# Performance work log

Measured on AMD Instinct MI355X. Metric: run time of the kernel, lower is better.

Reference implementation:

```python
import jax, jax.numpy as jnp
import numpy as np
from jax import lax

B, T, D, U = 128, 1024, 256, 48


def setup_inputs() -> dict:
    key = jax.random.key(0)
    k1, k2, k3 = jax.random.split(key, 3)
    x = jax.random.normal(k1, (B, T, D), dtype=jnp.float32)
    kernel = jax.random.normal(k2, (D, U), dtype=jnp.float32) * (1.0 / np.sqrt(D))
    bias = jnp.zeros((U,), dtype=jnp.float32)
    chain_kernel = jax.random.normal(k3, (U, U), dtype=jnp.float32)
    return {"x": x, "kernel": kernel, "bias": bias, "chain_kernel": chain_kernel}


def _viterbi_decode(logits, trans):
    # logits: [B, T, U], trans: [U, U]; full-length sequences (mask=None)
    init_state = logits[:, 0]  # [B, U]
    steps = jnp.swapaxes(logits[:, 1:], 0, 1)  # [T-1, B, U]

    def fwd(state, logit_t):
        # scores[b, i, j] = state[b, i] + trans[i, j]
        scores = state[:, :, None] + trans[None]  # [B, U, U]
        bp = jnp.argmax(scores, axis=1)            # [B, U] best prev tag
        new_state = logit_t + jnp.max(scores, axis=1)
        return new_state, bp

    final_state, bps = lax.scan(fwd, init_state, steps)  # bps: [T-1, B, U]
    last_tag = jnp.argmax(final_state, axis=-1)          # [B]

    def back(tag, bp):
        prev = jnp.take_along_axis(bp, tag[:, None], axis=1)[:, 0]
        return prev, prev

    # reverse scan emits tags for t = 0..T-2 in forward time order
    _, tags_head = lax.scan(back, last_tag, bps, reverse=True)  # [T-1, B]
    tags = jnp.concatenate([tags_head, last_tag[None]], axis=0)  # [T, B]
    return jnp.transpose(tags)  # [B, T]


def reference(x, kernel, bias, chain_kernel):
    # _dense_layer: linear activation -> x @ kernel + bias
    logits = jnp.einsum('btd,du->btu', x, kernel) + bias  # [B, T, U]
    pred_ids = _viterbi_decode(logits, chain_kernel)       # [B, T] int
    return pred_ids.astype(jnp.float32)
```

## Files before the change

### kernel.cpp

```cpp
#include <hip/hip_runtime.h>
#include <cstdint>

#define B_ 128
#define T_ 1024
#define D_ 256
#define U_ 48

typedef float v2f __attribute__((ext_vector_type(2)));

__device__ __forceinline__ v2f pk_add(v2f a, v2f b) {
    v2f d;
    asm("v_pk_add_f32 %0, %1, %2" : "=v"(d) : "v"(a), "v"(b));
    return d;
}
__device__ __forceinline__ float max3f(float a, float b, float c) {
    float d;
    asm("v_max3_f32 %0, %1, %2, %3" : "=v"(d) : "v"(a), "v"(b), "v"(c));
    return d;
}

__global__ __launch_bounds__(256, 1) void k_logits(const float* __restrict__ x,
                                                   const float* __restrict__ kern,
                                                   const float* __restrict__ bias,
                                                   float* __restrict__ logits) {
    __shared__ float K[D_ * U_];
    __shared__ float bsh[U_];
    const int tid = threadIdx.x;
    for (int i = tid; i < D_ * U_; i += 256) K[i] = kern[i];
    if (tid < U_) bsh[tid] = bias[tid];
    __syncthreads();

    const long row0 = (long)blockIdx.x * 256 + tid;
    const long row1 = row0 + (long)B_ * T_ / 2;
    const float4* xr0 = (const float4*)(x + row0 * D_);
    const float4* xr1 = (const float4*)(x + row1 * D_);

    float a0[U_], a1[U_];
#pragma unroll
    for (int u = 0; u < U_; ++u) { a0[u] = 0.0f; a1[u] = 0.0f; }

#pragma unroll 1
    for (int blk = 0; blk < D_ / 32; ++blk) {
        float4 xa[8], xb[8];
#pragma unroll
        for (int i = 0; i < 8; ++i) xa[i] = xr0[blk * 8 + i];
#pragma unroll
        for (int i = 0; i < 8; ++i) xb[i] = xr1[blk * 8 + i];

#pragma unroll
        for (int i = 0; i < 8; ++i) {
            const int d4 = blk * 8 + i;
            const float xc0[4] = {xa[i].x, xa[i].y, xa[i].z, xa[i].w};
            const float xc1[4] = {xb[i].x, xb[i].y, xb[i].z, xb[i].w};
#pragma unroll
            for (int c = 0; c < 4; ++c) {
                const float4* kp = (const float4*)&K[(d4 * 4 + c) * U_];
                const float s0 = xc0[c], s1 = xc1[c];
#pragma unroll
                for (int u4 = 0; u4 < U_ / 4; ++u4) {
                    float4 kv = kp[u4];
                    a0[u4*4+0] += s0 * kv.x;  a1[u4*4+0] += s1 * kv.x;
                    a0[u4*4+1] += s0 * kv.y;  a1[u4*4+1] += s1 * kv.y;
                    a0[u4*4+2] += s0 * kv.z;  a1[u4*4+2] += s1 * kv.z;
                    a0[u4*4+3] += s0 * kv.w;  a1[u4*4+3] += s1 * kv.w;
                }
            }
        }
    }

    float4* o0 = (float4*)(logits + row0 * U_);
    float4* o1 = (float4*)(logits + row1 * U_);
#pragma unroll
    for (int i = 0; i < U_ / 4; ++i) {
        float4 v0, v1;
        v0.x = a0[i*4+0] + bsh[i*4+0];  v1.x = a1[i*4+0] + bsh[i*4+0];
        v0.y = a0[i*4+1] + bsh[i*4+1];  v1.y = a1[i*4+1] + bsh[i*4+1];
        v0.z = a0[i*4+2] + bsh[i*4+2];  v1.z = a1[i*4+2] + bsh[i*4+2];
        v0.w = a0[i*4+3] + bsh[i*4+3];  v1.w = a1[i*4+3] + bsh[i*4+3];
        o0[i] = v0;
        o1[i] = v1;
    }
}

__device__ __forceinline__ float step_max_lds(const float4* sb, const v2f* tc2) {
    float4 s[12];
#pragma unroll
    for (int k = 0; k < 12; ++k) s[k] = sb[k];
    float cf[48];
#pragma unroll
    for (int k = 0; k < 12; ++k) {
        v2f lo, hi;
        lo.x = s[k].x; lo.y = s[k].y;
        hi.x = s[k].z; hi.y = s[k].w;
        v2f r0 = pk_add(lo, tc2[2 * k + 0]);
        v2f r1 = pk_add(hi, tc2[2 * k + 1]);
        cf[4*k+0] = r0.x; cf[4*k+1] = r0.y;
        cf[4*k+2] = r1.x; cf[4*k+3] = r1.y;
    }
    float t1[16];
#pragma unroll
    for (int i = 0; i < 16; ++i) t1[i] = max3f(cf[3*i], cf[3*i+1], cf[3*i+2]);
    float t2[6];
#pragma unroll
    for (int i = 0; i < 5; ++i) t2[i] = max3f(t1[3*i], t1[3*i+1], t1[3*i+2]);
    t2[5] = t1[15];
    const float a = max3f(t2[0], t2[1], t2[2]);
    const float b = max3f(t2[3], t2[4], t2[5]);
    return fmaxf(a, b);
}

__global__ __launch_bounds__(64, 1) void k_forward(const float* __restrict__ trans,
                                                   const float* __restrict__ logits,
                                                   float* __restrict__ delta) {
    __shared__ float4 sbuf[2][U_ / 4];
    const int lane = threadIdx.x;
    const int b = blockIdx.x;
    const int u = (lane < U_) ? lane : (U_ - 1);

    v2f tc2[U_ / 2];
#pragma unroll
    for (int v = 0; v < U_; v += 2) {
        tc2[v / 2].x = trans[v * U_ + u];
        tc2[v / 2].y = trans[(v + 1) * U_ + u];
    }

    const float* lin = logits + (long)b * T_ * U_;
    float* dout = delta + (long)b * T_ * U_;

    float state = lin[u];
    dout[u] = state;
    ((float*)sbuf[0])[u] = state;

    float pf[8];
#pragma unroll
    for (int i = 0; i < 8; ++i) pf[i] = lin[(1 + i) * U_ + u];

    const float* lp = lin + 9 * U_ + u;
    float* dp = dout + 1 * U_ + u;

#pragma unroll 1
    for (int g = 0; g < 127; ++g) {
#pragma unroll
        for (int j = 0; j < 8; ++j) {
            const float logit = pf[j];
            pf[j] = lp[j * U_];

            const float4* sb = sbuf[j & 1];
            const float m = step_max_lds(sb, tc2);
            state = logit + m;
            ((float*)sbuf[(j & 1) ^ 1])[u] = state;
            dp[j * U_] = state;
        }
        lp += 8 * U_;
        dp += 8 * U_;
    }

#pragma unroll
    for (int j = 0; j < 7; ++j) {
        const float logit = pf[j];
        const float4* sb = sbuf[j & 1];
        const float m = step_max_lds(sb, tc2);
        state = logit + m;
        ((float*)sbuf[(j & 1) ^ 1])[u] = state;
        dp[j * U_] = state;
    }
}

__global__ __launch_bounds__(64, 1) void k_forward_inplace(const float* __restrict__ trans,
                                                           float* __restrict__ delta) {
    __shared__ float4 sbuf[2][U_ / 4];
    const int lane = threadIdx.x;
    const int b = blockIdx.x;
    const int u = (lane < U_) ? lane : (U_ - 1);

    v2f tc2[U_ / 2];
#pragma unroll
    for (int v = 0; v < U_; v += 2) {
        tc2[v / 2].x = trans[v * U_ + u];
        tc2[v / 2].y = trans[(v + 1) * U_ + u];
    }

    float* base = delta + (long)b * T_ * U_;
    float state = base[u];
    ((float*)sbuf[0])[u] = state;

#pragma unroll 1
    for (int t = 1; t < T_; ++t) {
        const float logit = base[(long)t * U_ + u];
        const float m = step_max_lds(sbuf[(t - 1) & 1], tc2);
        state = logit + m;
        ((float*)sbuf[t & 1])[u] = state;
        base[(long)t * U_ + u] = state;
    }
}

#define BP_ROWS 32
__global__ __launch_bounds__(64, 1) void k_bp(const float* __restrict__ trans,
                                              const float* __restrict__ delta,
                                              unsigned char* __restrict__ bp) {
    __shared__ float sbuf[2][U_];
    const int lane = threadIdx.x;
    const int u = (lane < U_) ? lane : (U_ - 1);

    float tc[U_];
#pragma unroll
    for (int v = 0; v < U_; ++v) tc[v] = trans[v * U_ + u];

    const int NROW = B_ * (T_ - 1);
    const int row0 = blockIdx.x * BP_ROWS;
    if (row0 >= NROW) return;

    int b = row0 / (T_ - 1);
    int tm1 = row0 - b * (T_ - 1);

    float dval = delta[((long)b * T_ + tm1) * U_ + u];

#pragma unroll 1
    for (int i = 0; i < BP_ROWS; ++i) {
        const int row = row0 + i;
        if (row >= NROW) break;

        sbuf[i & 1][u] = dval;

        int bn = b, tn = tm1 + 1;
        if (tn == T_ - 1) { tn = 0; bn = b + 1; }
        float dnext = 0.0f;
        if (row + 1 < NROW) dnext = delta[((long)bn * T_ + tn) * U_ + u];

        const float4* sb4 = (const float4*)sbuf[i & 1];
        float best = -3.4e38f;
        int bi = 0;
#pragma unroll
        for (int k = 0; k < U_ / 4; ++k) {
            float4 s = sb4[k];
            float c0 = s.x + tc[4*k+0];
            float c1 = s.y + tc[4*k+1];
            float c2 = s.z + tc[4*k+2];
            float c3 = s.w + tc[4*k+3];
            bi = (c0 > best) ? 4*k+0 : bi;  best = fmaxf(best, c0);
            bi = (c1 > best) ? 4*k+1 : bi;  best = fmaxf(best, c1);
            bi = (c2 > best) ? 4*k+2 : bi;  best = fmaxf(best, c2);
            bi = (c3 > best) ? 4*k+3 : bi;  best = fmaxf(best, c3);
        }
        bp[(long)row * U_ + u] = (unsigned char)bi;

        b = bn; tm1 = tn; dval = dnext;
    }
}

#define KB_ 32
#define NB_ 32
__global__ __launch_bounds__(256) void k_back(const float* __restrict__ delta,
                                              const unsigned char* __restrict__ bp,
                                              float* __restrict__ out) {
    __shared__ unsigned char bpl[1024 * U_];
    __shared__ unsigned char gmap[NB_ * U_];
    __shared__ unsigned char eIn[NB_];
    __shared__ float tags[T_];
    __shared__ int Ash;
    const int tid = threadIdx.x;
    const int b = blockIdx.x;

    const uint32_t* src = (const uint32_t*)(bp + (long)b * (T_ - 1) * U_);
    uint32_t* dst = (uint32_t*)bpl;
    const int NW = (T_ - 1) * U_ / 4;
    for (int i = tid; i < NW; i += 256) dst[i] = src[i];
    if (tid < U_) bpl[1023 * U_ + tid] = (unsigned char)tid;

    if (tid < 64) {
        const int lane = tid;
        float v = (lane < U_) ? delta[((long)b * T_ + (T_ - 1)) * U_ + lane] : -3.4e38f;
        int idx = (lane < U_) ? lane : 64;
#pragma unroll
        for (int off = 32; off >= 1; off >>= 1) {
            const float ov = __shfl_xor(v, off);
            const int oi = __shfl_xor(idx, off);
            if (ov > v || (ov == v && oi < idx)) { v = ov; idx = oi; }
        }
        if (lane == 0) Ash = idx;
    }
    __syncthreads();

    int ik[6], ek[6], ck[6];
#pragma unroll
    for (int k = 0; k < 6; ++k) {
        const int tau = tid + k * 256;
        ik[k] = tau / U_;
        ek[k] = tau - ik[k] * U_;
        ck[k] = ek[k];
    }
#pragma unroll
    for (int h = 0; h < KB_; ++h) {
#pragma unroll
        for (int k = 0; k < 6; ++k) {
            const int r = ik[k] * KB_ + (KB_ - 1 - h);
            ck[k] = bpl[r * U_ + ck[k]];
        }
    }
#pragma unroll
    for (int k = 0; k < 6; ++k) gmap[ik[k] * U_ + ek[k]] = (unsigned char)ck[k];
    __syncthreads();

    if (tid == 0) {
        int cur = Ash;
        eIn[NB_ - 1] = (unsigned char)cur;
#pragma unroll 1
        for (int i = NB_ - 1; i >= 1; --i) {
            cur = gmap[i * U_ + cur];
            eIn[i - 1] = (unsigned char)cur;
        }
    }
    __syncthreads();

    if (tid < NB_) {
        const int i = tid;
        int cur = eIn[i];
#pragma unroll
        for (int h = 0; h < KB_; ++h) {
            const int r = i * KB_ + (KB_ - 1 - h);
            cur = bpl[r * U_ + cur];
            tags[r] = (float)cur;
        }
    }
    __syncthreads();

    float* o = out + (long)b * T_;
    for (int i = tid; i < T_; i += 256) o[i] = tags[i];
}

extern "C" void kernel_launch(void* const* d_in, const int* in_sizes, int n_in,
                              void* d_out, int out_size, void* d_ws, size_t ws_size,
                              hipStream_t stream) {
    const float* x     = (const float*)d_in[0];
    const float* kern  = (const float*)d_in[1];
    const float* bias  = (const float*)d_in[2];
    const float* trans = (const float*)d_in[3];
    float* out = (float*)d_out;

    const size_t NBT = (size_t)B_ * T_ * U_ * sizeof(float);

    float* logits = (float*)d_ws;
    const bool two_buf = ws_size >= 2 * NBT + (size_t)B_ * T_ * U_;
    float* delta = two_buf ? (float*)((char*)d_ws + NBT) : logits;
    unsigned char* bp = (unsigned char*)d_ws + (two_buf ? 2 * NBT : NBT);

    const int NROW = B_ * (T_ - 1);
    const int bp_grid = (NROW + BP_ROWS - 1) / BP_ROWS;

    k_logits<<<(B_ * T_ / 2) / 256, 256, 0, stream>>>(x, kern, bias, logits);
    if (two_buf)
        k_forward<<<B_, 64, 0, stream>>>(trans, logits, delta);
    else
        k_forward_inplace<<<B_, 64, 0, stream>>>(trans, logits);
    k_bp  <<<bp_grid, 64, 0, stream>>>(trans, delta, bp);
    k_back<<<B_, 256, 0, stream>>>(delta, bp, out);
}
```

Measured before the change: 500.4 us.

## Fuse forward recursion, backpointer computation and backtrace into one kernel

Replaces the separate forward, backpointer and backtrace kernels with one kernel per batch row. One wavefront runs the max-plus recursion and writes states into a 64-row LDS ring buffer, while a second wavefront computes argmax backpointers for the previous 32-step batch straight into LDS. This removes the global delta and bp round trips and two launches. The cost is a block barrier every 32 steps on the serial chain and only 128 blocks with 128 threads each doing the backpointer work.

Result: slower. 689.2 us (+37.7%).

```diff
diff --git a/kernel.cpp b/kernel.cpp
--- a/kernel.cpp
+++ b/kernel.cpp
@@ -109,167 +109,122 @@
     return fmaxf(a, b);
 }
 
-__global__ __launch_bounds__(64, 1) void k_forward(const float* __restrict__ trans,
-                                                   const float* __restrict__ logits,
-                                                   float* __restrict__ delta) {
-    __shared__ float4 sbuf[2][U_ / 4];
-    const int lane = threadIdx.x;
+#define RING 64
+#define BATCH 32
+
+#define CHAIN_STEP(IDX, J, DOPF)                                            \
+    {                                                                       \
+        const float logit = pf[IDX];                                        \
+        if (DOPF) pf[IDX] = lp[(J) * U_];                                   \
+        const float m = step_max_lds((const float4*)(ringf + roff), tc2);   \
+        state = logit + m;                                                  \
+        uint32_t woff = roff + U_;                                          \
+        woff = (woff >= (uint32_t)(RING * U_)) ? 0u : woff;                 \
+        ringf[woff + u] = state;                                            \
+        roff = woff;                                                        \
+    }
+
+#define CHAIN_GROUP8(PHI, DOPF)                                             \
+    CHAIN_STEP(((PHI) + 0) & 7, 0, DOPF)                                    \
+    CHAIN_STEP(((PHI) + 1) & 7, 1, DOPF)                                    \
+    CHAIN_STEP(((PHI) + 2) & 7, 2, DOPF)                                    \
+    CHAIN_STEP(((PHI) + 3) & 7, 3, DOPF)                                    \
+    CHAIN_STEP(((PHI) + 4) & 7, 4, DOPF)                                    \
+    CHAIN_STEP(((PHI) + 5) & 7, 5, DOPF)                                    \
+    CHAIN_STEP(((PHI) + 6) & 7, 6, DOPF)                                    \
+    CHAIN_STEP(((PHI) + 7) & 7, 7, DOPF)                                    \
+    lp += 8 * U_;
+
+__global__ __launch_bounds__(128, 1) void k_fused(const float* __restrict__ trans,
+                                                  const float* __restrict__ logits,
+                                                  float* __restrict__ out) {
+    __shared__ float ringf[RING * U_];
+    __shared__ unsigned char bpl[1024 * U_];
+    __shared__ unsigned char gmap[32 * U_];
+    __shared__ unsigned char eIn[32];
+    __shared__ int Ash;
+
+    const int tid = threadIdx.x;
+    const int wid = tid >> 6;
+    const int lane = tid & 63;
     const int b = blockIdx.x;
     const int u = (lane < U_) ? lane : (U_ - 1);
 
+    const float* lin = logits + (long)b * T_ * U_;
+
     v2f tc2[U_ / 2];
-#pragma unroll
-    for (int v = 0; v < U_; v += 2) {
-        tc2[v / 2].x = trans[v * U_ + u];
-        tc2[v / 2].y = trans[(v + 1) * U_ + u];
-    }
-
-    const float* lin = logits + (long)b * T_ * U_;
-    float* dout = delta + (long)b * T_ * U_;
-
-    float state = lin[u];
-    dout[u] = state;
-    ((float*)sbuf[0])[u] = state;
-
-    float pf[8];
-#pragma unroll
-    for (int i = 0; i < 8; ++i) pf[i] = lin[(1 + i) * U_ + u];
-
+    float state = 0.0f, pf[8];
     const float* lp = lin + 9 * U_ + u;
-    float* dp = dout + 1 * U_ + u;
-
-#pragma unroll 1
-    for (int g = 0; g < 127; ++g) {
-#pragma unroll
-        for (int j = 0; j < 8; ++j) {
-            const float logit = pf[j];
-            pf[j] = lp[j * U_];
-
-            const float4* sb = sbuf[j & 1];
-            const float m = step_max_lds(sb, tc2);
-            state = logit + m;
-            ((float*)sbuf[(j & 1) ^ 1])[u] = state;
-            dp[j * U_] = state;
-        }
-        lp += 8 * U_;
-        dp += 8 * U_;
-    }
-
-#pragma unroll
-    for (int j = 0; j < 7; ++j) {
-        const float logit = pf[j];
-        const float4* sb = sbuf[j & 1];
-        const float m = step_max_lds(sb, tc2);
-        state = logit + m;
-        ((float*)sbuf[(j & 1) ^ 1])[u] = state;
-        dp[j * U_] = state;
-    }
-}
-
-__global__ __launch_bounds__(64, 1) void k_forward_inplace(const float* __restrict__ trans,
-                                                           float* __restrict__ delta) {
-    __shared__ float4 sbuf[2][U_ / 4];
-    const int lane = threadIdx.x;
-    const int b = blockIdx.x;
-    const int u = (lane < U_) ? lane : (U_ - 1);
-
-    v2f tc2[U_ / 2];
-#pragma unroll
-    for (int v = 0; v < U_; v += 2) {
-        tc2[v / 2].x = trans[v * U_ + u];
-        tc2[v / 2].y = trans[(v + 1) * U_ + u];
-    }
-
-    float* base = delta + (long)b * T_ * U_;
-    float state = base[u];
-    ((float*)sbuf[0])[u] = state;
-
-#pragma unroll 1
-    for (int t = 1; t < T_; ++t) {
-        const float logit = base[(long)t * U_ + u];
-        const float m = step_max_lds(sbuf[(t - 1) & 1], tc2);
-        state = logit + m;
-        ((float*)sbuf[t & 1])[u] = state;
-        base[(long)t * U_ + u] = state;
-    }
-}
-
-#define BP_ROWS 32
-__global__ __launch_bounds__(64, 1) void k_bp(const float* __restrict__ trans,
-                                              const float* __restrict__ delta,
-                                              unsigned char* __restrict__ bp) {
-    __shared__ float sbuf[2][U_];
-    const int lane = threadIdx.x;
-    const int u = (lane < U_) ? lane : (U_ - 1);
-
+    uint32_t roff = 0;
     float tc[U_];
-#pragma unroll
-    for (int v = 0; v < U_; ++v) tc[v] = trans[v * U_ + u];
-
-    const int NROW = B_ * (T_ - 1);
-    const int row0 = blockIdx.x * BP_ROWS;
-    if (row0 >= NROW) return;
-
-    int b = row0 / (T_ - 1);
-    int tm1 = row0 - b * (T_ - 1);
-
-    float dval = delta[((long)b * T_ + tm1) * U_ + u];
-
-#pragma unroll 1
-    for (int i = 0; i < BP_ROWS; ++i) {
-        const int row = row0 + i;
-        if (row >= NROW) break;
-
-        sbuf[i & 1][u] = dval;
-
-        int bn = b, tn = tm1 + 1;
-        if (tn == T_ - 1) { tn = 0; bn = b + 1; }
-        float dnext = 0.0f;
-        if (row + 1 < NROW) dnext = delta[((long)bn * T_ + tn) * U_ + u];
-
-        const float4* sb4 = (const float4*)sbuf[i & 1];
-        float best = -3.4e38f;
-        int bi = 0;
-#pragma unroll
-        for (int k = 0; k < U_ / 4; ++k) {
-            float4 s = sb4[k];
-            float c0 = s.x + tc[4*k+0];
-            float c1 = s.y + tc[4*k+1];
-            float c2 = s.z + tc[4*k+2];
-            float c3 = s.w + tc[4*k+3];
-            bi = (c0 > best) ? 4*k+0 : bi;  best = fmaxf(best, c0);
-            bi = (c1 > best) ? 4*k+1 : bi;  best = fmaxf(best, c1);
-            bi = (c2 > best) ? 4*k+2 : bi;  best = fmaxf(best, c2);
-            bi = (c3 > best) ? 4*k+3 : bi;  best = fmaxf(best, c3);
-        }
-        bp[(long)row * U_ + u] = (unsigned char)bi;
-
-        b = bn; tm1 = tn; dval = dnext;
-    }
-}
-
-#define KB_ 32
-#define NB_ 32
-__global__ __launch_bounds__(256) void k_back(const float* __restrict__ delta,
-                                              const unsigned char* __restrict__ bp,
-                                              float* __restrict__ out) {
-    __shared__ unsigned char bpl[1024 * U_];
-    __shared__ unsigned char gmap[NB_ * U_];
-    __shared__ unsigned char eIn[NB_];
-    __shared__ float tags[T_];
-    __shared__ int Ash;
-    const int tid = threadIdx.x;
-    const int b = blockIdx.x;
-
-    const uint32_t* src = (const uint32_t*)(bp + (long)b * (T_ - 1) * U_);
-    uint32_t* dst = (uint32_t*)bpl;
-    const int NW = (T_ - 1) * U_ / 4;
-    for (int i = tid; i < NW; i += 256) dst[i] = src[i];
+
+    if (wid == 0) {
+#pragma unroll
+        for (int v = 0; v < U_; v += 2) {
+            tc2[v / 2].x = trans[v * U_ + u];
+            tc2[v / 2].y = trans[(v + 1) * U_ + u];
+        }
+        state = lin[u];
+        ringf[u] = state;
+#pragma unroll
+        for (int i = 0; i < 8; ++i) pf[i] = lin[(1 + i) * U_ + u];
+
+        CHAIN_GROUP8(0, 1)
+        CHAIN_GROUP8(0, 1)
+        CHAIN_GROUP8(0, 1)
+        CHAIN_STEP(0, 0, 1) CHAIN_STEP(1, 1, 1) CHAIN_STEP(2, 2, 1)
+        CHAIN_STEP(3, 3, 1) CHAIN_STEP(4, 4, 1) CHAIN_STEP(5, 5, 1)
+        CHAIN_STEP(6, 6, 1)
+        lp += 7 * U_;
+    } else {
+#pragma unroll
+        for (int v = 0; v < U_; ++v) tc[v] = trans[v * U_ + u];
+    }
+    __syncthreads();
+
+#pragma unroll 1
+    for (int kb = 1; kb <= 32; ++kb) {
+        if (wid == 0 && kb <= 31) {
+            if (kb < 31) {
+                CHAIN_GROUP8(7, 1) CHAIN_GROUP8(7, 1)
+                CHAIN_GROUP8(7, 1) CHAIN_GROUP8(7, 1)
+            } else {
+                CHAIN_GROUP8(7, 1) CHAIN_GROUP8(7, 1)
+                CHAIN_GROUP8(7, 1) CHAIN_GROUP8(7, 0)
+            }
+        }
+        if (wid == 1) {
+            const int kbp = kb - 1;
+            const int r0 = kbp * BATCH;
+            const int nr = (kbp == 31) ? (BATCH - 1) : BATCH;
+            uint32_t boff = (uint32_t)((r0 & (RING - 1)) * U_);
+#pragma unroll 1
+            for (int i = 0; i < nr; ++i) {
+                const float4* sb4 = (const float4*)(ringf + boff);
+                float best = -3.4e38f;
+                int bi = 0;
+#pragma unroll
+                for (int k = 0; k < U_ / 4; ++k) {
+                    float4 s = sb4[k];
+                    float c0 = s.x + tc[4*k+0];
+                    float c1 = s.y + tc[4*k+1];
+                    float c2 = s.z + tc[4*k+2];
+                    float c3 = s.w + tc[4*k+3];
+                    bi = (c0 > best) ? 4*k+0 : bi;  best = fmaxf(best, c0);
+                    bi = (c1 > best) ? 4*k+1 : bi;  best = fmaxf(best, c1);
+                    bi = (c2 > best) ? 4*k+2 : bi;  best = fmaxf(best, c2);
+                    bi = (c3 > best) ? 4*k+3 : bi;  best = fmaxf(best, c3);
+                }
+                bpl[(r0 + i) * U_ + u] = (unsigned char)bi;
+                boff += U_;
+            }
+        }
+        __syncthreads();
+    }
+
     if (tid < U_) bpl[1023 * U_ + tid] = (unsigned char)tid;
-
-    if (tid < 64) {
-        const int lane = tid;
-        float v = (lane < U_) ? delta[((long)b * T_ + (T_ - 1)) * U_ + lane] : -3.4e38f;
+    if (wid == 0) {
+        float v = (lane < U_) ? ringf[(1023 & (RING - 1)) * U_ + lane] : -3.4e38f;
         int idx = (lane < U_) ? lane : 64;
 #pragma unroll
         for (int off = 32; off >= 1; off >>= 1) {
@@ -281,51 +236,47 @@
     }
     __syncthreads();
 
-    int ik[6], ek[6], ck[6];
-#pragma unroll
-    for (int k = 0; k < 6; ++k) {
-        const int tau = tid + k * 256;
+    int ik[12], ek[12], ck[12];
+#pragma unroll
+    for (int k = 0; k < 12; ++k) {
+        const int tau = tid + k * 128;
         ik[k] = tau / U_;
         ek[k] = tau - ik[k] * U_;
         ck[k] = ek[k];
     }
 #pragma unroll
-    for (int h = 0; h < KB_; ++h) {
-#pragma unroll
-        for (int k = 0; k < 6; ++k) {
-            const int r = ik[k] * KB_ + (KB_ - 1 - h);
+    for (int h = 0; h < 32; ++h) {
+#pragma unroll
+        for (int k = 0; k < 12; ++k) {
+            const int r = ik[k] * 32 + (31 - h);
             ck[k] = bpl[r * U_ + ck[k]];
         }
     }
 #pragma unroll
-    for (int k = 0; k < 6; ++k) gmap[ik[k] * U_ + ek[k]] = (unsigned char)ck[k];
+    for (int k = 0; k < 12; ++k) gmap[ik[k] * U_ + ek[k]] = (unsigned char)ck[k];
     __syncthreads();
 
     if (tid == 0) {
         int cur = Ash;
-        eIn[NB_ - 1] = (unsigned char)cur;
-#pragma unroll 1
-        for (int i = NB_ - 1; i >= 1; --i) {
+        eIn[31] = (unsigned char)cur;
+#pragma unroll 1
+        for (int i = 31; i >= 1; --i) {
             cur = gmap[i * U_ + cur];
             eIn[i - 1] = (unsigned char)cur;
         }
     }
     __syncthreads();
 
-    if (tid < NB_) {
-        const int i = tid;
-        int cur = eIn[i];
-#pragma unroll
-        for (int h = 0; h < KB_; ++h) {
-            const int r = i * KB_ + (KB_ - 1 - h);
+    float* o = out + (long)b * T_;
+    if (tid < 32) {
+        int cur = eIn[tid];
+#pragma unroll
+        for (int h = 0; h < 32; ++h) {
+            const int r = tid * 32 + (31 - h);
             cur = bpl[r * U_ + cur];
-            tags[r] = (float)cur;
-        }
-    }
-    __syncthreads();
-
-    float* o = out + (long)b * T_;
-    for (int i = tid; i < T_; i += 256) o[i] = tags[i];
+            o[r] = (float)cur;
+        }
+    }
 }
 
 extern "C" void kernel_launch(void* const* d_in, const int* in_sizes, int n_in,
@@ -337,21 +288,8 @@
     const float* trans = (const float*)d_in[3];
     float* out = (float*)d_out;
 
-    const size_t NBT = (size_t)B_ * T_ * U_ * sizeof(float);
-
     float* logits = (float*)d_ws;
-    const bool two_buf = ws_size >= 2 * NBT + (size_t)B_ * T_ * U_;
-    float* delta = two_buf ? (float*)((char*)d_ws + NBT) : logits;
-    unsigned char* bp = (unsigned char*)d_ws + (two_buf ? 2 * NBT : NBT);
-
-    const int NROW = B_ * (T_ - 1);
-    const int bp_grid = (NROW + BP_ROWS - 1) / BP_ROWS;
 
     k_logits<<<(B_ * T_ / 2) / 256, 256, 0, stream>>>(x, kern, bias, logits);
-    if (two_buf)
-        k_forward<<<B_, 64, 0, stream>>>(trans, logits, delta);
-    else
-        k_forward_inplace<<<B_, 64, 0, stream>>>(trans, logits);
-    k_bp  <<<bp_grid, 64, 0, stream>>>(trans, delta, bp);
-    k_back<<<B_, 256, 0, stream>>>(delta, bp, out);
-}
+    k_fused <<<B_, 128, 0, stream>>>(trans, logits, out);
+}
```

## Retile logits GEMM as 8-row by 12-column register tiles per thread

Applied to the files above, without the earlier changes.

Restructures the dense-layer kernel so each thread computes an 8-row by 12-unit output tile instead of 2 full rows of 48 units. Four lanes share a row group and split the units, which cuts LDS reads of the kernel matrix per FMA and lowers per-thread register pressure. The grid shrinks to 512 rows per block. Global x loads now stride 8 rows per lane, so coalescing changes and four lanes read duplicate x data.

Result: no change. 499.2 us (-0.2%).

```diff
diff --git a/kernel.cpp b/kernel.cpp
--- a/kernel.cpp
+++ b/kernel.cpp
@@ -30,55 +30,60 @@
     if (tid < U_) bsh[tid] = bias[tid];
     __syncthreads();
 
-    const long row0 = (long)blockIdx.x * 256 + tid;
-    const long row1 = row0 + (long)B_ * T_ / 2;
-    const float4* xr0 = (const float4*)(x + row0 * D_);
-    const float4* xr1 = (const float4*)(x + row1 * D_);
-
-    float a0[U_], a1[U_];
-#pragma unroll
-    for (int u = 0; u < U_; ++u) { a0[u] = 0.0f; a1[u] = 0.0f; }
-
-#pragma unroll 1
-    for (int blk = 0; blk < D_ / 32; ++blk) {
-        float4 xa[8], xb[8];
-#pragma unroll
-        for (int i = 0; i < 8; ++i) xa[i] = xr0[blk * 8 + i];
-#pragma unroll
-        for (int i = 0; i < 8; ++i) xb[i] = xr1[blk * 8 + i];
-
-#pragma unroll
-        for (int i = 0; i < 8; ++i) {
-            const int d4 = blk * 8 + i;
-            const float xc0[4] = {xa[i].x, xa[i].y, xa[i].z, xa[i].w};
-            const float xc1[4] = {xb[i].x, xb[i].y, xb[i].z, xb[i].w};
-#pragma unroll
-            for (int c = 0; c < 4; ++c) {
-                const float4* kp = (const float4*)&K[(d4 * 4 + c) * U_];
-                const float s0 = xc0[c], s1 = xc1[c];
-#pragma unroll
-                for (int u4 = 0; u4 < U_ / 4; ++u4) {
-                    float4 kv = kp[u4];
-                    a0[u4*4+0] += s0 * kv.x;  a1[u4*4+0] += s1 * kv.x;
-                    a0[u4*4+1] += s0 * kv.y;  a1[u4*4+1] += s1 * kv.y;
-                    a0[u4*4+2] += s0 * kv.z;  a1[u4*4+2] += s1 * kv.z;
-                    a0[u4*4+3] += s0 * kv.w;  a1[u4*4+3] += s1 * kv.w;
-                }
+    const int lane = tid & 63;
+    const int wv = tid >> 6;
+    const int ug = lane >> 4;
+    const int u0 = ug * 12;
+    const int rs = lane & 15;
+    const long row0 = (long)blockIdx.x * 512 + (long)wv * 128 + (long)rs * 8;
+    const float* xb = x + row0 * D_;
+
+    float acc[8][12];
+#pragma unroll
+    for (int r = 0; r < 8; ++r)
+#pragma unroll
+        for (int j = 0; j < 12; ++j) acc[r][j] = 0.0f;
+
+#pragma unroll 1
+    for (int d4 = 0; d4 < D_ / 4; ++d4) {
+        float4 xv[8];
+#pragma unroll
+        for (int r = 0; r < 8; ++r)
+            xv[r] = *(const float4*)(xb + r * D_ + d4 * 4);
+#pragma unroll
+        for (int c = 0; c < 4; ++c) {
+            const float4* kp = (const float4*)&K[(d4 * 4 + c) * U_ + u0];
+            const float4 k0 = kp[0];
+            const float4 k1 = kp[1];
+            const float4 k2 = kp[2];
+#pragma unroll
+            for (int r = 0; r < 8; ++r) {
+                const float s = (c == 0) ? xv[r].x : (c == 1) ? xv[r].y
+                              : (c == 2) ? xv[r].z : xv[r].w;
+                acc[r][0]  += s * k0.x;  acc[r][1]  += s * k0.y;
+                acc[r][2]  += s * k0.z;  acc[r][3]  += s * k0.w;
+                acc[r][4]  += s * k1.x;  acc[r][5]  += s * k1.y;
+                acc[r][6]  += s * k1.z;  acc[r][7]  += s * k1.w;
+                acc[r][8]  += s * k2.x;  acc[r][9]  += s * k2.y;
+                acc[r][10] += s * k2.z;  acc[r][11] += s * k2.w;
             }
         }
     }
 
-    float4* o0 = (float4*)(logits + row0 * U_);
-    float4* o1 = (float4*)(logits + row1 * U_);
-#pragma unroll
-    for (int i = 0; i < U_ / 4; ++i) {
-        float4 v0, v1;
-        v0.x = a0[i*4+0] + bsh[i*4+0];  v1.x = a1[i*4+0] + bsh[i*4+0];
-        v0.y = a0[i*4+1] + bsh[i*4+1];  v1.y = a1[i*4+1] + bsh[i*4+1];
-        v0.z = a0[i*4+2] + bsh[i*4+2];  v1.z = a1[i*4+2] + bsh[i*4+2];
-        v0.w = a0[i*4+3] + bsh[i*4+3];  v1.w = a1[i*4+3] + bsh[i*4+3];
-        o0[i] = v0;
-        o1[i] = v1;
+    const float b0 = bsh[u0+0], b1 = bsh[u0+1], b2  = bsh[u0+2],  b3  = bsh[u0+3];
+    const float b4 = bsh[u0+4], b5 = bsh[u0+5], b6  = bsh[u0+6],  b7  = bsh[u0+7];
+    const float b8 = bsh[u0+8], b9 = bsh[u0+9], b10 = bsh[u0+10], b11 = bsh[u0+11];
+#pragma unroll
+    for (int r = 0; r < 8; ++r) {
+        float4* op = (float4*)(logits + (row0 + r) * U_ + u0);
+        float4 v0, v1, v2;
+        v0.x = acc[r][0] + b0;   v0.y = acc[r][1] + b1;
+        v0.z = acc[r][2] + b2;   v0.w = acc[r][3] + b3;
+        v1.x = acc[r][4] + b4;   v1.y = acc[r][5] + b5;
+        v1.z = acc[r][6] + b6;   v1.w = acc[r][7] + b7;
+        v2.x = acc[r][8] + b8;   v2.y = acc[r][9] + b9;
+        v2.z = acc[r][10] + b10; v2.w = acc[r][11] + b11;
+        op[0] = v0; op[1] = v1; op[2] = v2;
     }
 }
 
@@ -347,7 +352,7 @@
     const int NROW = B_ * (T_ - 1);
     const int bp_grid = (NROW + BP_ROWS - 1) / BP_ROWS;
 
-    k_logits<<<(B_ * T_ / 2) / 256, 256, 0, stream>>>(x, kern, bias, logits);
+    k_logits<<<B_ * T_ / 512, 256, 0, stream>>>(x, kern, bias, logits);
     if (two_buf)
         k_forward<<<B_, 64, 0, stream>>>(trans, logits, delta);
     else
```
